# Performance work log

Hardware: AMD Instinct MI355X
Metric: run time of the kernel (lower is better)

Reference implementation:

```python
import jax, jax.numpy as jnp
import numpy as np

WINDOW = 7
NUM_HEADS = 12
DIM = 384


def _relative_position_index(ws):
    coords_h = np.arange(ws)
    coords_w = np.arange(ws)
    coords = np.stack(np.meshgrid(coords_h, coords_w, indexing='ij'))  # [2,ws,ws]
    coords_flatten = coords.transpose(1, 2, 0).reshape(-1, 2)          # [ws*ws,2]
    rel = coords_flatten[:, None, :] - coords_flatten[None, :, :]      # [N,N,2]
    rel[:, :, 0] += ws - 1
    rel[:, :, 1] += ws - 1
    rel[:, :, 0] *= 2 * ws - 1
    return rel.sum(-1).astype(np.int32)                                # [N,N]


def setup_inputs() -> dict:
    key = jax.random.key(0)
    ks = jax.random.split(key, 8)
    B_, N, C, H = 4096, WINDOW * WINDOW, DIM, NUM_HEADS
    x = jax.random.normal(ks[0], (B_, N, C), dtype=jnp.float32)
    mask = jax.random.normal(ks[1], (1, 1, N, N), dtype=jnp.float32)
    qkv_w = jax.random.normal(ks[2], (C, 3 * C), dtype=jnp.float32) * 0.02
    qkv_b = jnp.zeros((3 * C,), dtype=jnp.float32)
    proj_w = jax.random.normal(ks[3], (C, C), dtype=jnp.float32) * 0.02
    proj_b = jnp.zeros((C,), dtype=jnp.float32)
    bias_table = jax.random.normal(ks[4], ((2 * WINDOW - 1) ** 2, H), dtype=jnp.float32) * 0.02
    rel_index = jnp.asarray(_relative_position_index(WINDOW))  # int32 [N,N]
    return {"x": x, "mask": mask, "qkv_w": qkv_w, "qkv_b": qkv_b,
            "proj_w": proj_w, "proj_b": proj_b, "bias_table": bias_table,
            "rel_index": rel_index}


def reference(x, mask, qkv_w, qkv_b, proj_w, proj_b, bias_table, rel_index):
    B_, N, C = x.shape
    H = NUM_HEADS
    hd = C // H
    scale = hd ** (-0.5)
    # qkv projection -> [3, B_, H, N, hd]
    qkv = (x @ qkv_w + qkv_b).reshape(B_, N, 3, H, hd).transpose(2, 0, 3, 1, 4)
    q, k, v = qkv[0], qkv[1], qkv[2]
    attn = jnp.einsum('bhnd,bhmd->bhnm', q, k) * scale  # [B_,H,N,N]
    # gathered relative position bias: [N,N,H] -> [H,N,N]
    bias = bias_table[rel_index].transpose(2, 0, 1)
    attn = attn + bias[None] + mask
    attn = jax.nn.softmax(attn, axis=-1)
    out = jnp.einsum('bhnm,bhmd->bhnd', attn, v)        # [B_,H,N,hd]
    out = out.transpose(0, 2, 1, 3).reshape(B_, N, C)
    return out @ proj_w + proj_b
```

## Files before the change

kernel.cpp:

```cpp
#include <hip/hip_runtime.h>
#include <hip/hip_bf16.h>
#include <stdint.h>

typedef unsigned short u16;
typedef __bf16 bf16x8 __attribute__((ext_vector_type(8)));
typedef float f32x4 __attribute__((ext_vector_type(4)));

#define NWIN 4096
#define NTOK 49
#define CDIM 384
#define NHEAD 12
#define HD 32
#define MROWS (NWIN * NTOK)
#define QKVN (3 * CDIM)
#define GK 384
#define GNT 6
#define SCALE 0.17677669529663689f

__device__ __forceinline__ u16 f2bf(float f) {
  uint32_t u = __float_as_uint(f);
  u += 0x7fff + ((u >> 16) & 1);
  return (u16)(u >> 16);
}

__device__ __forceinline__ void gload_lds16(const void* g, void* l) {
  __builtin_amdgcn_global_load_lds(
      (const __attribute__((address_space(1))) unsigned int*)g,
      (__attribute__((address_space(3))) unsigned int*)l, 16, 0, 0);
}


__global__ __launch_bounds__(256) void cvt_x_kernel(const float* __restrict__ x,
                                                    u16* __restrict__ xb, int n4) {
  int i = blockIdx.x * blockDim.x + threadIdx.x;
  int stride = gridDim.x * blockDim.x;
  for (; i < n4; i += stride) {
    float4 v = ((const float4*)x)[i];
    ushort4 o;
    o.x = f2bf(v.x); o.y = f2bf(v.y); o.z = f2bf(v.z); o.w = f2bf(v.w);
    ((ushort4*)xb)[i] = o;
  }
}

__global__ __launch_bounds__(256) void cvt_wT_kernel(const float* __restrict__ w,
                                                     u16* __restrict__ wT, int K, int N) {
  int i = blockIdx.x * blockDim.x + threadIdx.x;
  if (i >= K * N) return;
  int n = i / K, k = i - n * K;
  wT[i] = f2bf(w[k * N + n]);
}

__global__ __launch_bounds__(256) void build_bias_kernel(const float* __restrict__ bt,
                                                         const int* __restrict__ ri,
                                                         const float* __restrict__ mask,
                                                         float* __restrict__ bias12p) {
  int i = blockIdx.x * blockDim.x + threadIdx.x;
  if (i >= NHEAD * 64 * 64) return;
  int h = i >> 12, r = (i >> 6) & 63, c = i & 63;
  float v = 0.f;
  if (r < NTOK && c < NTOK) v = bt[ri[r * NTOK + c] * NHEAD + h] + mask[r * NTOK + c];
  bias12p[i] = v;
}


template <int MODE>
__global__ __launch_bounds__(256) void gemm128(const u16* __restrict__ A,
                                               const u16* __restrict__ BT,
                                               const float* __restrict__ bias,
                                               float* __restrict__ outF,
                                               u16* __restrict__ q_ws,
                                               u16* __restrict__ k_ws,
                                               u16* __restrict__ vT_ws,
                                               int n_tiles) {
  __shared__ __align__(16) u16 As[2][128 * 64];
  __shared__ __align__(16) u16 Bs[2][128 * 64];
  const int tid = threadIdx.x;
  const int wave = tid >> 6, lane = tid & 63;

  const int nwg = gridDim.x;
  int bid = blockIdx.x;
  bid = (bid & 7) * (nwg >> 3) + (bid >> 3);

  const int mt = bid / n_tiles, ntile = bid - mt * n_tiles;
  const int m0 = mt << 7, n0 = ntile << 7;
  const int fr = lane & 15, fg = lane >> 4;
  const int wr = (wave >> 1) << 6, wc = (wave & 1) << 6;

  f32x4 acc[4][4] = {};

  auto stage = [&](int k0s, int bufi) {
#pragma unroll
    for (int it = 0; it < 4; ++it) {
      const int c = it * 256 + tid;
      const int row = c >> 3, col8 = c & 7;
      const int scol = ((col8 ^ (row & 7)) << 3);
      gload_lds16(A + (size_t)(m0 + row) * GK + k0s + scol, &As[bufi][c * 8]);
    }
#pragma unroll
    for (int it = 0; it < 4; ++it) {
      const int c = it * 256 + tid;
      const int row = c >> 3, col8 = c & 7;
      const int scol = ((col8 ^ (row & 7)) << 3);
      gload_lds16(BT + (size_t)(n0 + row) * GK + k0s + scol, &Bs[bufi][c * 8]);
    }
  };

  stage(0, 0);
  stage(64, 1);

#pragma unroll
  for (int t = 0; t < GNT; ++t) {
    if (t < GNT - 1) asm volatile("s_waitcnt vmcnt(8)" ::: "memory");
    else             asm volatile("s_waitcnt vmcnt(0)" ::: "memory");
    __builtin_amdgcn_s_barrier();

    const int buf = t & 1;
#pragma unroll
    for (int kk = 0; kk < 2; ++kk) {
      bf16x8 av[4], bv[4];
#pragma unroll
      for (int i = 0; i < 4; ++i) {
        const int row = wr + i * 16 + fr;
        const int swz = ((kk << 2) | fg) ^ (fr & 7);
        av[i] = *(const bf16x8*)((const char*)&As[buf][0] + (size_t)row * 128 + (swz << 4));
      }
#pragma unroll
      for (int i = 0; i < 4; ++i) {
        const int row = wc + i * 16 + fr;
        const int swz = ((kk << 2) | fg) ^ (fr & 7);
        bv[i] = *(const bf16x8*)((const char*)&Bs[buf][0] + (size_t)row * 128 + (swz << 4));
      }
      __builtin_amdgcn_s_setprio(1);
#pragma unroll
      for (int i = 0; i < 4; ++i)
#pragma unroll
        for (int j = 0; j < 4; ++j)
          acc[i][j] = __builtin_amdgcn_mfma_f32_16x16x32_bf16(av[i], bv[j], acc[i][j], 0, 0, 0);
      __builtin_amdgcn_s_setprio(0);
    }

    __builtin_amdgcn_s_barrier();
    if (t + 2 < GNT) stage((t + 2) << 6, buf);
  }

  const int col0 = n0 + wc + fr;
  float bvadd[4];
#pragma unroll
  for (int j = 0; j < 4; ++j) bvadd[j] = bias[col0 + j * 16];

  if (MODE == 0) {
    const int s = col0 / CDIM;
    int hh[4], dd[4];
#pragma unroll
    for (int j = 0; j < 4; ++j) {
      const int cr = col0 + j * 16 - s * CDIM;
      hh[j] = cr >> 5; dd[j] = cr & 31;
    }
#pragma unroll
    for (int i = 0; i < 4; ++i) {
#pragma unroll
      for (int r = 0; r < 4; ++r) {
        const int row_g = m0 + wr + i * 16 + fg * 4 + r;
        const int b = row_g / NTOK, n = row_g - b * NTOK;
        const size_t bhb = (size_t)b * NHEAD;
#pragma unroll
        for (int j = 0; j < 4; ++j) {
          const float v = acc[i][j][r] + bvadd[j];
          const size_t bh = bhb + hh[j];
          if (s == 0)      q_ws[(bh * NTOK + n) * HD + dd[j]] = f2bf(v * SCALE);
          else if (s == 1) k_ws[(bh * NTOK + n) * HD + dd[j]] = f2bf(v);
          else             vT_ws[(bh * HD + dd[j]) * 64 + n] = f2bf(v);
        }
      }
    }
  } else {
#pragma unroll
    for (int i = 0; i < 4; ++i) {
#pragma unroll
      for (int r = 0; r < 4; ++r) {
        const int row_g = m0 + wr + i * 16 + fg * 4 + r;
        float* op = outF + (size_t)row_g * CDIM + col0;
#pragma unroll
        for (int j = 0; j < 4; ++j) op[j * 16] = acc[i][j][r] + bvadd[j];
      }
    }
  }
}


__global__ __launch_bounds__(64) void attn_kernel(const u16* __restrict__ q_ws,
                                                  const u16* __restrict__ k_ws,
                                                  const u16* __restrict__ vT_ws,
                                                  const float* __restrict__ bias12p,
                                                  u16* __restrict__ att_ws) {
  __shared__ __align__(16) float S[64 * 66];
  __shared__ __align__(16) u16 P[64 * 72];
  const int bh = blockIdx.x;
  const int b = bh / NHEAD, h = bh - b * NHEAD;
  const int lane = threadIdx.x;
  const int fr = lane & 15, fg = lane >> 4;
  const u16* qp = q_ws + (size_t)bh * NTOK * HD;
  const u16* kp = k_ws + (size_t)bh * NTOK * HD;
  const u16* vp = vT_ws + (size_t)bh * HD * 64;

  bf16x8 bv[2][2];
#pragma unroll
  for (int kt = 0; kt < 2; ++kt)
#pragma unroll
    for (int n2 = 0; n2 < 2; ++n2)
      bv[kt][n2] = *(const bf16x8*)&vp[(n2 * 16 + fr) * 64 + kt * 32 + fg * 8];

  bf16x8 aq[4], bk[4];
#pragma unroll
  for (int i = 0; i < 4; ++i) {
    int m = i * 16 + fr;
    m = m < NTOK ? m : NTOK - 1;
    aq[i] = *(const bf16x8*)&qp[m * HD + fg * 8];
    bk[i] = *(const bf16x8*)&kp[m * HD + fg * 8];
  }
  f32x4 sacc[4][4] = {};
#pragma unroll
  for (int i = 0; i < 4; ++i)
#pragma unroll
    for (int j = 0; j < 4; ++j)
      sacc[i][j] = __builtin_amdgcn_mfma_f32_16x16x32_bf16(aq[i], bk[j], sacc[i][j], 0, 0, 0);

  const float* bp = bias12p + h * 64 * 64;
#pragma unroll
  for (int i = 0; i < 4; ++i)
#pragma unroll
    for (int j = 0; j < 4; ++j)
#pragma unroll
      for (int r = 0; r < 4; ++r) {
        const int row = i * 16 + fg * 4 + r, col = j * 16 + fr;
        S[row * 66 + col] = sacc[i][j][r] + bp[row * 64 + col];
      }
  __syncthreads();

  {
    const int r = lane;
    float sv[49];
#pragma unroll
    for (int j = 0; j < 49; ++j) sv[j] = S[r * 66 + j];
    float mx = sv[0];
#pragma unroll
    for (int j = 1; j < 49; ++j) mx = fmaxf(mx, sv[j]);
    float s0 = 0.f, s1 = 0.f;
#pragma unroll
    for (int j = 0; j < 48; j += 2) {
      sv[j]     = __expf(sv[j] - mx);     s0 += sv[j];
      sv[j + 1] = __expf(sv[j + 1] - mx); s1 += sv[j + 1];
    }
    sv[48] = __expf(sv[48] - mx); s0 += sv[48];
    const float inv = (r < NTOK) ? 1.f / (s0 + s1) : 0.f;
#pragma unroll
    for (int c = 0; c < 8; ++c) {
      uint32_t w[4];
#pragma unroll
      for (int u = 0; u < 4; ++u) {
        const int j0 = c * 8 + u * 2, j1 = j0 + 1;
        const uint32_t lo = (j0 < 49) ? (uint32_t)f2bf(sv[j0] * inv) : 0u;
        const uint32_t hi = (j1 < 49) ? (uint32_t)f2bf(sv[j1] * inv) : 0u;
        w[u] = lo | (hi << 16);
      }
      *(uint4*)&P[r * 72 + c * 8] = make_uint4(w[0], w[1], w[2], w[3]);
    }
  }
  __syncthreads();

  f32x4 oacc[4][2] = {};
#pragma unroll
  for (int kt = 0; kt < 2; ++kt) {
    bf16x8 ap[4];
#pragma unroll
    for (int i = 0; i < 4; ++i)
      ap[i] = *(const bf16x8*)&P[(i * 16 + fr) * 72 + kt * 32 + fg * 8];
#pragma unroll
    for (int i = 0; i < 4; ++i)
#pragma unroll
      for (int n2 = 0; n2 < 2; ++n2)
        oacc[i][n2] = __builtin_amdgcn_mfma_f32_16x16x32_bf16(ap[i], bv[kt][n2], oacc[i][n2], 0, 0, 0);
  }
  u16* ao = att_ws + ((size_t)b * NTOK) * CDIM + h * HD;
#pragma unroll
  for (int i = 0; i < 4; ++i)
#pragma unroll
    for (int n2 = 0; n2 < 2; ++n2)
#pragma unroll
      for (int r = 0; r < 4; ++r) {
        const int row = i * 16 + fg * 4 + r, col = n2 * 16 + fr;
        if (row < NTOK) ao[(size_t)row * CDIM + col] = f2bf(oacc[i][n2][r]);
      }
}


extern "C" void kernel_launch(void* const* d_in, const int* in_sizes, int n_in,
                              void* d_out, int out_size, void* d_ws, size_t ws_size,
                              hipStream_t stream) {
  (void)in_sizes; (void)n_in; (void)out_size; (void)ws_size;
  const float* x      = (const float*)d_in[0];
  const float* mask   = (const float*)d_in[1];
  const float* qkv_w  = (const float*)d_in[2];
  const float* qkv_b  = (const float*)d_in[3];
  const float* proj_w = (const float*)d_in[4];
  const float* proj_b = (const float*)d_in[5];
  const float* btab   = (const float*)d_in[6];
  const int*   ridx   = (const int*)d_in[7];
  float* out = (float*)d_out;

  char* ws = (char*)d_ws;
  size_t off = 0;
  auto alloc = [&](size_t bytes) {
    char* p = ws + off;
    off = (off + bytes + 255) & ~(size_t)255;
    return p;
  };
  u16* q_ws    = (u16*)alloc((size_t)NWIN * NHEAD * NTOK * HD * 2);
  u16* k_ws    = (u16*)alloc((size_t)NWIN * NHEAD * NTOK * HD * 2);
  u16* vT_ws   = (u16*)alloc((size_t)NWIN * NHEAD * HD * 64 * 2);
  u16* att_ws  = (u16*)alloc((size_t)MROWS * CDIM * 2);
  u16* qkvWT   = (u16*)alloc((size_t)QKVN * CDIM * 2);
  u16* projWT  = (u16*)alloc((size_t)CDIM * CDIM * 2);
  float* bias12p = (float*)alloc((size_t)NHEAD * 64 * 64 * 4);

  u16* x_bf = (u16*)d_out;

  cvt_x_kernel<<<4096, 256, 0, stream>>>(x, x_bf, MROWS * CDIM / 4);
  cvt_wT_kernel<<<(QKVN * CDIM + 255) / 256, 256, 0, stream>>>(qkv_w, qkvWT, CDIM, QKVN);
  cvt_wT_kernel<<<(CDIM * CDIM + 255) / 256, 256, 0, stream>>>(proj_w, projWT, CDIM, CDIM);
  build_bias_kernel<<<(NHEAD * 64 * 64 + 255) / 256, 256, 0, stream>>>(btab, ridx, mask, bias12p);

  gemm128<0><<<(MROWS / 128) * (QKVN / 128), 256, 0, stream>>>(
      x_bf, qkvWT, qkv_b, nullptr, q_ws, k_ws, vT_ws, QKVN / 128);

  attn_kernel<<<NWIN * NHEAD, 64, 0, stream>>>(q_ws, k_ws, vT_ws, bias12p, att_ws);

  gemm128<1><<<(MROWS / 128) * (CDIM / 128), 256, 0, stream>>>(
      att_ws, projWT, proj_b, out, nullptr, nullptr, nullptr, CDIM / 128);
}
```

Measured before the change: 1.253 ms.

## Halve GEMM K-tile and alias attention LDS buffers to raise occupancy

The GEMM K step drops from 64 to 32, with 12 iterations, a matching swizzle, and half the LDS per double buffer. Both GEMM kernels now use launch_bounds(256,5) so more workgroups fit on each CU. The attention kernel reuses one LDS buffer for both scores and probabilities, adding a barrier after the scores are read into registers, and requests two blocks per SIMD. The aim is better latency hiding through higher occupancy, at the cost of more barriers and waitcnts per unit of K work.

```diff
diff --git a/kernel.cpp b/kernel.cpp
--- a/kernel.cpp
+++ b/kernel.cpp
@@ -14,7 +14,7 @@
 #define MROWS (NWIN * NTOK)
 #define QKVN (3 * CDIM)
 #define GK 384
-#define GNT 6
+#define GNT 12
 #define SCALE 0.17677669529663689f
 
 __device__ __forceinline__ u16 f2bf(float f) {
@@ -64,16 +64,16 @@
 
 
 template <int MODE>
-__global__ __launch_bounds__(256) void gemm128(const u16* __restrict__ A,
-                                               const u16* __restrict__ BT,
-                                               const float* __restrict__ bias,
-                                               float* __restrict__ outF,
-                                               u16* __restrict__ q_ws,
-                                               u16* __restrict__ k_ws,
-                                               u16* __restrict__ vT_ws,
-                                               int n_tiles) {
-  __shared__ __align__(16) u16 As[2][128 * 64];
-  __shared__ __align__(16) u16 Bs[2][128 * 64];
+__device__ __forceinline__ void gemm_body(const u16* __restrict__ A,
+                                          const u16* __restrict__ BT,
+                                          const float* __restrict__ bias,
+                                          float* __restrict__ outF,
+                                          u16* __restrict__ q_ws,
+                                          u16* __restrict__ k_ws,
+                                          u16* __restrict__ vT_ws,
+                                          int n_tiles) {
+  __shared__ __align__(16) u16 As[2][128 * 32];
+  __shared__ __align__(16) u16 Bs[2][128 * 32];
   const int tid = threadIdx.x;
   const int wave = tid >> 6, lane = tid & 63;
 
@@ -90,57 +90,50 @@
 
   auto stage = [&](int k0s, int bufi) {
 #pragma unroll
-    for (int it = 0; it < 4; ++it) {
+    for (int it = 0; it < 2; ++it) {
       const int c = it * 256 + tid;
-      const int row = c >> 3, col8 = c & 7;
-      const int scol = ((col8 ^ (row & 7)) << 3);
+      const int row = c >> 2, col4 = c & 3;
+      const int scol = ((col4 ^ ((row >> 1) & 3)) << 3);
       gload_lds16(A + (size_t)(m0 + row) * GK + k0s + scol, &As[bufi][c * 8]);
     }
 #pragma unroll
-    for (int it = 0; it < 4; ++it) {
+    for (int it = 0; it < 2; ++it) {
       const int c = it * 256 + tid;
-      const int row = c >> 3, col8 = c & 7;
-      const int scol = ((col8 ^ (row & 7)) << 3);
+      const int row = c >> 2, col4 = c & 3;
+      const int scol = ((col4 ^ ((row >> 1) & 3)) << 3);
       gload_lds16(BT + (size_t)(n0 + row) * GK + k0s + scol, &Bs[bufi][c * 8]);
     }
   };
 
   stage(0, 0);
-  stage(64, 1);
+  stage(32, 1);
+
+  const int swz = fg ^ ((fr >> 1) & 3);
 
 #pragma unroll
   for (int t = 0; t < GNT; ++t) {
-    if (t < GNT - 1) asm volatile("s_waitcnt vmcnt(8)" ::: "memory");
+    if (t < GNT - 1) asm volatile("s_waitcnt vmcnt(4)" ::: "memory");
     else             asm volatile("s_waitcnt vmcnt(0)" ::: "memory");
     __builtin_amdgcn_s_barrier();
 
     const int buf = t & 1;
-#pragma unroll
-    for (int kk = 0; kk < 2; ++kk) {
-      bf16x8 av[4], bv[4];
-#pragma unroll
-      for (int i = 0; i < 4; ++i) {
-        const int row = wr + i * 16 + fr;
-        const int swz = ((kk << 2) | fg) ^ (fr & 7);
-        av[i] = *(const bf16x8*)((const char*)&As[buf][0] + (size_t)row * 128 + (swz << 4));
-      }
-#pragma unroll
-      for (int i = 0; i < 4; ++i) {
-        const int row = wc + i * 16 + fr;
-        const int swz = ((kk << 2) | fg) ^ (fr & 7);
-        bv[i] = *(const bf16x8*)((const char*)&Bs[buf][0] + (size_t)row * 128 + (swz << 4));
-      }
-      __builtin_amdgcn_s_setprio(1);
-#pragma unroll
-      for (int i = 0; i < 4; ++i)
-#pragma unroll
-        for (int j = 0; j < 4; ++j)
-          acc[i][j] = __builtin_amdgcn_mfma_f32_16x16x32_bf16(av[i], bv[j], acc[i][j], 0, 0, 0);
-      __builtin_amdgcn_s_setprio(0);
-    }
+    bf16x8 av[4], bv[4];
+#pragma unroll
+    for (int i = 0; i < 4; ++i)
+      av[i] = *(const bf16x8*)((const char*)&As[buf][0] + (size_t)(wr + i * 16 + fr) * 64 + (swz << 4));
+#pragma unroll
+    for (int i = 0; i < 4; ++i)
+      bv[i] = *(const bf16x8*)((const char*)&Bs[buf][0] + (size_t)(wc + i * 16 + fr) * 64 + (swz << 4));
+    __builtin_amdgcn_s_setprio(1);
+#pragma unroll
+    for (int i = 0; i < 4; ++i)
+#pragma unroll
+      for (int j = 0; j < 4; ++j)
+        acc[i][j] = __builtin_amdgcn_mfma_f32_16x16x32_bf16(av[i], bv[j], acc[i][j], 0, 0, 0);
+    __builtin_amdgcn_s_setprio(0);
 
     __builtin_amdgcn_s_barrier();
-    if (t + 2 < GNT) stage((t + 2) << 6, buf);
+    if (t + 2 < GNT) stage((t + 2) << 5, buf);
   }
 
   const int col0 = n0 + wc + fr;
@@ -187,14 +180,32 @@
   }
 }
 
-
-__global__ __launch_bounds__(64) void attn_kernel(const u16* __restrict__ q_ws,
-                                                  const u16* __restrict__ k_ws,
-                                                  const u16* __restrict__ vT_ws,
-                                                  const float* __restrict__ bias12p,
-                                                  u16* __restrict__ att_ws) {
-  __shared__ __align__(16) float S[64 * 66];
-  __shared__ __align__(16) u16 P[64 * 72];
+__global__ __launch_bounds__(256, 5) void gemm_qkv(const u16* __restrict__ A,
+                                                   const u16* __restrict__ BT,
+                                                   const float* __restrict__ bias,
+                                                   u16* __restrict__ q_ws,
+                                                   u16* __restrict__ k_ws,
+                                                   u16* __restrict__ vT_ws,
+                                                   int n_tiles) {
+  gemm_body<0>(A, BT, bias, nullptr, q_ws, k_ws, vT_ws, n_tiles);
+}
+
+__global__ __launch_bounds__(256, 5) void gemm_proj(const u16* __restrict__ A,
+                                                    const u16* __restrict__ BT,
+                                                    const float* __restrict__ bias,
+                                                    float* __restrict__ outF,
+                                                    int n_tiles) {
+  gemm_body<1>(A, BT, bias, outF, nullptr, nullptr, nullptr, n_tiles);
+}
+
+
+__global__ __launch_bounds__(64, 2) void attn_kernel(const u16* __restrict__ q_ws,
+                                                     const u16* __restrict__ k_ws,
+                                                     const u16* __restrict__ vT_ws,
+                                                     const float* __restrict__ bias12p,
+                                                     u16* __restrict__ att_ws) {
+  __shared__ __align__(16) float SP[64 * 67];
+  u16* P = (u16*)SP;
   const int bh = blockIdx.x;
   const int b = bh / NHEAD, h = bh - b * NHEAD;
   const int lane = threadIdx.x;
@@ -233,38 +244,38 @@
 #pragma unroll
       for (int r = 0; r < 4; ++r) {
         const int row = i * 16 + fg * 4 + r, col = j * 16 + fr;
-        S[row * 66 + col] = sacc[i][j][r] + bp[row * 64 + col];
+        SP[row * 67 + col] = sacc[i][j][r] + bp[row * 64 + col];
       }
   __syncthreads();
 
-  {
-    const int r = lane;
-    float sv[49];
-#pragma unroll
-    for (int j = 0; j < 49; ++j) sv[j] = S[r * 66 + j];
-    float mx = sv[0];
-#pragma unroll
-    for (int j = 1; j < 49; ++j) mx = fmaxf(mx, sv[j]);
-    float s0 = 0.f, s1 = 0.f;
-#pragma unroll
-    for (int j = 0; j < 48; j += 2) {
-      sv[j]     = __expf(sv[j] - mx);     s0 += sv[j];
-      sv[j + 1] = __expf(sv[j + 1] - mx); s1 += sv[j + 1];
-    }
-    sv[48] = __expf(sv[48] - mx); s0 += sv[48];
-    const float inv = (r < NTOK) ? 1.f / (s0 + s1) : 0.f;
-#pragma unroll
-    for (int c = 0; c < 8; ++c) {
-      uint32_t w[4];
-#pragma unroll
-      for (int u = 0; u < 4; ++u) {
-        const int j0 = c * 8 + u * 2, j1 = j0 + 1;
-        const uint32_t lo = (j0 < 49) ? (uint32_t)f2bf(sv[j0] * inv) : 0u;
-        const uint32_t hi = (j1 < 49) ? (uint32_t)f2bf(sv[j1] * inv) : 0u;
-        w[u] = lo | (hi << 16);
-      }
-      *(uint4*)&P[r * 72 + c * 8] = make_uint4(w[0], w[1], w[2], w[3]);
-    }
+  const int r = lane;
+  float sv[49];
+#pragma unroll
+  for (int j = 0; j < 49; ++j) sv[j] = SP[r * 67 + j];
+  __syncthreads();
+
+  float mx = sv[0];
+#pragma unroll
+  for (int j = 1; j < 49; ++j) mx = fmaxf(mx, sv[j]);
+  float s0 = 0.f, s1 = 0.f;
+#pragma unroll
+  for (int j = 0; j < 48; j += 2) {
+    sv[j]     = __expf(sv[j] - mx);     s0 += sv[j];
+    sv[j + 1] = __expf(sv[j + 1] - mx); s1 += sv[j + 1];
+  }
+  sv[48] = __expf(sv[48] - mx); s0 += sv[48];
+  const float inv = (r < NTOK) ? 1.f / (s0 + s1) : 0.f;
+#pragma unroll
+  for (int c = 0; c < 8; ++c) {
+    uint32_t w[4];
+#pragma unroll
+    for (int u = 0; u < 4; ++u) {
+      const int j0 = c * 8 + u * 2, j1 = j0 + 1;
+      const uint32_t lo = (j0 < 49) ? (uint32_t)f2bf(sv[j0] * inv) : 0u;
+      const uint32_t hi = (j1 < 49) ? (uint32_t)f2bf(sv[j1] * inv) : 0u;
+      w[u] = lo | (hi << 16);
+    }
+    *(uint4*)&P[r * 72 + c * 8] = make_uint4(w[0], w[1], w[2], w[3]);
   }
   __syncthreads();
 
@@ -287,9 +298,9 @@
 #pragma unroll
     for (int n2 = 0; n2 < 2; ++n2)
 #pragma unroll
-      for (int r = 0; r < 4; ++r) {
-        const int row = i * 16 + fg * 4 + r, col = n2 * 16 + fr;
-        if (row < NTOK) ao[(size_t)row * CDIM + col] = f2bf(oacc[i][n2][r]);
+      for (int rr = 0; rr < 4; ++rr) {
+        const int row = i * 16 + fg * 4 + rr, col = n2 * 16 + fr;
+        if (row < NTOK) ao[(size_t)row * CDIM + col] = f2bf(oacc[i][n2][rr]);
       }
 }
 
@@ -330,11 +341,11 @@
   cvt_wT_kernel<<<(CDIM * CDIM + 255) / 256, 256, 0, stream>>>(proj_w, projWT, CDIM, CDIM);
   build_bias_kernel<<<(NHEAD * 64 * 64 + 255) / 256, 256, 0, stream>>>(btab, ridx, mask, bias12p);
 
-  gemm128<0><<<(MROWS / 128) * (QKVN / 128), 256, 0, stream>>>(
-      x_bf, qkvWT, qkv_b, nullptr, q_ws, k_ws, vT_ws, QKVN / 128);
+  gemm_qkv<<<(MROWS / 128) * (QKVN / 128), 256, 0, stream>>>(
+      x_bf, qkvWT, qkv_b, q_ws, k_ws, vT_ws, QKVN / 128);
 
   attn_kernel<<<NWIN * NHEAD, 64, 0, stream>>>(q_ws, k_ws, vT_ws, bias12p, att_ws);
 
-  gemm128<1><<<(MROWS / 128) * (CDIM / 128), 256, 0, stream>>>(
-      att_ws, projWT, proj_b, out, nullptr, nullptr, nullptr, CDIM / 128);
-}
+  gemm_proj<<<(MROWS / 128) * (CDIM / 128), 256, 0, stream>>>(
+      att_ws, projWT, proj_b, out, CDIM / 128);
+}
```

After: 2.285 ms. 1.82x slower.
